# Performance work log

Hardware: AMD Instinct MI355X
Metric: run time of the kernel (lower is better)

The kernel has to match this reference:

```python
import jax, jax.numpy as jnp
import numpy as np

N, D, H, E, TOPK = 4096, 1024, 2048, 8, 2
EPS = 1e-10

def setup_inputs() -> dict:
    key = jax.random.key(0)
    ks = jax.random.split(key, 6)
    s = 0.02  # init scale for weights
    return {
        "x": jax.random.normal(ks[0], (N, D), dtype=jnp.float32),
        "gates": jax.random.uniform(ks[1], (N, E), dtype=jnp.float32),
        "W1": (jax.random.normal(ks[2], (E, D, H), dtype=jnp.float32) * s),
        "b1": jnp.zeros((E, H), dtype=jnp.float32),
        "W2": (jax.random.normal(ks[3], (E, H, H // 2), dtype=jnp.float32) * s),
        "b2": jnp.zeros((E, H // 2), dtype=jnp.float32),
        "W3": (jax.random.normal(ks[4], (E, H // 2, 1), dtype=jnp.float32) * s),
        "b3": jnp.zeros((E, 1), dtype=jnp.float32),
    }

def reference(x, gates, W1, b1, W2, b2, W3, b3):
    num_experts = gates.shape[1]
    # top-k gate masking + renormalization (matches MixtureOfExperts.call)
    _, topk_idx = jax.lax.top_k(gates, TOPK)              # [N, k]
    mask = jax.nn.one_hot(topk_idx, num_experts, dtype=gates.dtype).sum(axis=1)  # [N, E]
    g = gates * mask
    g = g / (g.sum(axis=-1, keepdims=True) + EPS)
    # Dense-masked expert computation. Mathematically identical to the
    # gather/split/segment-sum dispatch in SparseDispatcher: tokens with
    # zero gate for expert e contribute gate*sigmoid(...) = 0 in combine.
    # Dropout layers are identity at inference (training=False).
    h1 = jax.nn.relu(jnp.einsum('nd,edh->enh', x, W1) + b1[:, None, :])   # [E, N, H]
    h2 = jax.nn.relu(jnp.einsum('enh,ehg->eng', h1, W2) + b2[:, None, :]) # [E, N, H//2]
    y = jax.nn.sigmoid(jnp.einsum('eng,ego->eno', h2, W3) + b3[:, None, :])  # [E, N, 1]
    # combine: sum_e g[n,e] * y[e,n,:]  (== unsorted_segment_sum over dispatched rows)
    prediction = jnp.einsum('ne,eno->no', g, y)  # [N, 1]
    return prediction, g
```

## Files before the change

kernel.cpp:

```cpp
#include <hip/hip_runtime.h>
#include <hip/hip_bf16.h>
#include <math.h>

#define NTOK 4096
#define DIN  1024
#define H1D  2048
#define H2D  1024
#define NE   8
#define KSEL 2

constexpr int BM = 128, BN = 128, BK = 32;
constexpr int MAX_TILES = NTOK / BM;

typedef __attribute__((ext_vector_type(8))) __bf16 bf16x8;
typedef __attribute__((ext_vector_type(4))) float  f32x4;

__device__ __forceinline__ ushort f2bf(float f) {
    union { float f; unsigned u; } c; c.f = f;
    unsigned u = c.u;
    return (ushort)((u + 0x7fffu + ((u >> 16) & 1u)) >> 16);
}

__global__ void zero_counts(int* counts) {
    if (threadIdx.x < NE) counts[threadIdx.x] = 0;
}

__global__ void convert_x(const float* __restrict__ x, ushort* __restrict__ xbf) {
    int i = (blockIdx.x * blockDim.x + threadIdx.x) * 4;
    float4 v = *(const float4*)(x + i);
    ushort4 o;
    o.x = f2bf(v.x); o.y = f2bf(v.y); o.z = f2bf(v.z); o.w = f2bf(v.w);
    *(ushort4*)(xbf + i) = o;
}

__global__ __launch_bounds__(256)
void transpose_cvt(const float* __restrict__ W, ushort* __restrict__ Wt,
                   int K, int N) {
    __shared__ float t[64][132];
    const int e  = blockIdx.z;
    const int n0 = blockIdx.x * 128;
    const int k0 = blockIdx.y * 64;
    const int tid = threadIdx.x;

    const float* src = W + ((size_t)e * K + k0) * N + n0;
#pragma unroll
    for (int p = 0; p < 8; ++p) {
        int c  = tid + p * 256;
        int kk = c >> 5;
        int nn = (c & 31) * 4;
        float4 v = *(const float4*)(src + (size_t)kk * N + nn);
        t[kk][nn + 0] = v.x; t[kk][nn + 1] = v.y;
        t[kk][nn + 2] = v.z; t[kk][nn + 3] = v.w;
    }
    __syncthreads();

    const int n = tid >> 1;
    const int h = tid & 1;
    ushort outv[32];
#pragma unroll
    for (int j = 0; j < 32; ++j) outv[j] = f2bf(t[h * 32 + j][n]);
    ushort* dst = Wt + ((size_t)e * N + n0 + n) * K + k0 + h * 32;
#pragma unroll
    for (int q = 0; q < 4; ++q)
        *(uint4*)(dst + q * 8) = *(const uint4*)(outv + q * 8);
}

__global__ void topk_gate(const float* __restrict__ gates,
                          float* __restrict__ g_out,
                          int* __restrict__ counts,
                          int* __restrict__ bucket,
                          int* __restrict__ tke,
                          float* __restrict__ tkg,
                          float* __restrict__ ppart)
{
    int n = blockIdx.x * blockDim.x + threadIdx.x;
    if (n >= NTOK) return;

    ppart[n * 2 + 0] = 0.f;
    ppart[n * 2 + 1] = 0.f;

    float v[NE];
#pragma unroll
    for (int e = 0; e < NE; ++e) v[e] = gates[n * NE + e];

    int i1 = 0; float v1 = v[0];
#pragma unroll
    for (int e = 1; e < NE; ++e) if (v[e] > v1) { v1 = v[e]; i1 = e; }
    int i2 = -1; float v2 = -1e30f;
#pragma unroll
    for (int e = 0; e < NE; ++e) if (e != i1 && v[e] > v2) { v2 = v[e]; i2 = e; }

    float s = v1 + v2 + 1e-10f;
    float g1 = v1 / s, g2 = v2 / s;

#pragma unroll
    for (int e = 0; e < NE; ++e) {
        float gv = 0.f;
        if (e == i1) gv = g1;
        if (e == i2) gv = g2;
        g_out[n * NE + e] = gv;
    }
    tke[n * 2 + 0] = i1; tkg[n * 2 + 0] = g1;
    tke[n * 2 + 1] = i2; tkg[n * 2 + 1] = g2;

    int s1 = atomicAdd(&counts[i1], 1);
    bucket[i1 * NTOK + s1] = n * 2 + 0;
    int s2 = atomicAdd(&counts[i2], 1);
    bucket[i2 * NTOK + s2] = n * 2 + 1;
}

template<int SHIFT, int MODE>
__global__ __launch_bounds__(256)
void moe_gemm(const ushort* __restrict__ Abf, int lda,
              const ushort* __restrict__ Wt,
              const float* __restrict__ bias,
              int N,
              const float* __restrict__ W3,
              ushort* __restrict__ Cbf,
              float* __restrict__ ppart,
              const int* __restrict__ bucket,
              const int* __restrict__ counts,
              int K)
{
    const int b    = blockIdx.x;
    const int e    = b & 7;
    const int idx  = b >> 3;
    const int tile = idx & (MAX_TILES - 1);
    const int col0 = (idx / MAX_TILES) * BN;

    const int cnt  = counts[e];
    const int row0 = tile * BM;
    if (row0 >= cnt) return;

    __shared__ int rowmap[BM];
    __shared__ __align__(16) ushort smA[2][BM * BK];
    __shared__ __align__(16) ushort smB[2][BN * BK];

    const int tid = threadIdx.x;
    if (tid < BM) {
        int r = row0 + tid;
        rowmap[tid] = (r < cnt) ? bucket[e * NTOK + r] : -1;
    }
    __syncthreads();

    const int lane = tid & 63;
    const int wid  = tid >> 6;
    const int wm   = wid >> 1;
    const int wn   = wid & 1;

    const ushort* aSrc[2];
    const ushort* bSrc[2];
    int dstOff[2];
#pragma unroll
    for (int i = 0; i < 2; ++i) {
        int c    = (wid * 2 + i) * 64 + lane;
        int line = c >> 2;
        int slot = c & 3;
        int sch  = slot ^ ((line >> 1) & 3);
        dstOff[i] = c * 8;
        int entry = rowmap[line];
        int arow  = (entry >= 0) ? (entry >> SHIFT) : 0;
        aSrc[i] = Abf + (size_t)arow * lda + sch * 8;
        bSrc[i] = Wt + ((size_t)e * N + col0 + line) * K + sch * 8;
    }

    f32x4 acc[4][4];
#pragma unroll
    for (int i = 0; i < 4; ++i)
#pragma unroll
        for (int j = 0; j < 4; ++j)
            acc[i][j] = (f32x4){0.f, 0.f, 0.f, 0.f};

    auto stage = [&](int buf, int k0) {
#pragma unroll
        for (int i = 0; i < 2; ++i)
            __builtin_amdgcn_global_load_lds(
                (const __attribute__((address_space(1))) unsigned*)(aSrc[i] + k0),
                (__attribute__((address_space(3))) unsigned*)&smA[buf][dstOff[i]],
                16, 0, 0);
#pragma unroll
        for (int i = 0; i < 2; ++i)
            __builtin_amdgcn_global_load_lds(
                (const __attribute__((address_space(1))) unsigned*)(bSrc[i] + k0),
                (__attribute__((address_space(3))) unsigned*)&smB[buf][dstOff[i]],
                16, 0, 0);
    };

    auto compute = [&](int buf) {
        bf16x8 a[4], bfr[4];
#pragma unroll
        for (int mi = 0; mi < 4; ++mi) {
            int row  = wm * 64 + mi * 16 + (lane & 15);
            int slot = (lane >> 4) ^ ((row >> 1) & 3);
            a[mi] = *(const bf16x8*)&smA[buf][row * 32 + slot * 8];
        }
#pragma unroll
        for (int ni = 0; ni < 4; ++ni) {
            int col  = wn * 64 + ni * 16 + (lane & 15);
            int slot = (lane >> 4) ^ ((col >> 1) & 3);
            bfr[ni] = *(const bf16x8*)&smB[buf][col * 32 + slot * 8];
        }
#pragma unroll
        for (int mi = 0; mi < 4; ++mi)
#pragma unroll
            for (int ni = 0; ni < 4; ++ni)
                acc[mi][ni] = __builtin_amdgcn_mfma_f32_16x16x32_bf16(
                    a[mi], bfr[ni], acc[mi][ni], 0, 0, 0);
    };

    const int nt = K / BK;
    stage(0, 0);
    __syncthreads();
    for (int t = 0; t < nt; ++t) {
        int cur = t & 1;
        if (t + 1 < nt) stage(cur ^ 1, (t + 1) * BK);
        compute(cur);
        __syncthreads();
    }

    if (MODE == 1) {
        float bb[4];
#pragma unroll
        for (int ni = 0; ni < 4; ++ni)
            bb[ni] = bias[e * N + col0 + wn * 64 + ni * 16 + (lane & 15)];
#pragma unroll
        for (int mi = 0; mi < 4; ++mi) {
#pragma unroll
            for (int r = 0; r < 4; ++r) {
                int rt = wm * 64 + mi * 16 + (lane >> 4) * 4 + r;
                int entry = rowmap[rt];
                if (entry < 0) continue;
                ushort* crow = Cbf + (size_t)entry * N + col0;
#pragma unroll
                for (int ni = 0; ni < 4; ++ni) {
                    float val = fmaxf(acc[mi][ni][r] + bb[ni], 0.f);
                    crow[wn * 64 + ni * 16 + (lane & 15)] = f2bf(val);
                }
            }
        }
    } else {
        float bb[4], w3l[4];
#pragma unroll
        for (int ni = 0; ni < 4; ++ni) {
            int cg = col0 + wn * 64 + ni * 16 + (lane & 15);
            bb[ni]  = bias[e * N + cg];
            w3l[ni] = W3[e * H2D + cg];
        }
#pragma unroll
        for (int mi = 0; mi < 4; ++mi) {
#pragma unroll
            for (int r = 0; r < 4; ++r) {
                float s = 0.f;
#pragma unroll
                for (int ni = 0; ni < 4; ++ni)
                    s += fmaxf(acc[mi][ni][r] + bb[ni], 0.f) * w3l[ni];
#pragma unroll
                for (int off = 1; off < 16; off <<= 1)
                    s += __shfl_xor(s, off, 16);
                if ((lane & 15) == 0) {
                    int rt = wm * 64 + mi * 16 + (lane >> 4) * 4 + r;
                    int entry = rowmap[rt];
                    if (entry >= 0) atomicAdd(&ppart[entry], s);
                }
            }
        }
    }
}

__global__ void finalize(const float* __restrict__ pp, const float* __restrict__ b3,
                         const int* __restrict__ tke, const float* __restrict__ tkg,
                         float* __restrict__ pred) {
    int n = blockIdx.x * blockDim.x + threadIdx.x;
    if (n >= NTOK) return;
    float r = 0.f;
#pragma unroll
    for (int k = 0; k < KSEL; ++k) {
        int p = n * 2 + k;
        int ee = tke[p];
        float y = 1.f / (1.f + expf(-(pp[p] + b3[ee])));
        r += tkg[p] * y;
    }
    pred[n] = r;
}

extern "C" void kernel_launch(void* const* d_in, const int* in_sizes, int n_in,
                              void* d_out, int out_size, void* d_ws, size_t ws_size,
                              hipStream_t stream)
{
    const float* x     = (const float*)d_in[0];
    const float* gates = (const float*)d_in[1];
    const float* W1    = (const float*)d_in[2];
    const float* b1    = (const float*)d_in[3];
    const float* W2    = (const float*)d_in[4];
    const float* b2    = (const float*)d_in[5];
    const float* W3    = (const float*)d_in[6];
    const float* b3    = (const float*)d_in[7];

    float* out  = (float*)d_out;
    float* pred = out;
    float* gout = out + NTOK;

    char* ws = (char*)d_ws;
    int*    counts = (int*)(ws);
    int*    bucket = (int*)(ws + 4096);
    int*    tke    = (int*)(ws + 4096 + 131072);
    float*  tkg    = (float*)(ws + 4096 + 131072 + 32768);
    float*  ppart  = (float*)(ws + 4096 + 131072 + 65536);
    ushort* xbf    = (ushort*)(ws + (1 << 20));
    ushort* h1bf   = (ushort*)(ws + (1 << 20) + (size_t)NTOK * DIN * 2);
    ushort* wtbuf  = (ushort*)(ws + (1 << 20) + (size_t)NTOK * DIN * 2
                                  + (size_t)NTOK * KSEL * H1D * 2);

    zero_counts<<<1, 64, 0, stream>>>(counts);
    topk_gate<<<NTOK / 256, 256, 0, stream>>>(gates, gout, counts, bucket,
                                              tke, tkg, ppart);
    convert_x<<<NTOK * DIN / 4 / 256, 256, 0, stream>>>(x, xbf);

    transpose_cvt<<<dim3(H1D / 128, DIN / 64, NE), 256, 0, stream>>>(
        W1, wtbuf, DIN, H1D);
    moe_gemm<1, 1><<<NE * (H1D / BN) * MAX_TILES, 256, 0, stream>>>(
        xbf, DIN, wtbuf, b1, H1D, nullptr, h1bf, nullptr, bucket, counts, DIN);

    transpose_cvt<<<dim3(H2D / 128, H1D / 64, NE), 256, 0, stream>>>(
        W2, wtbuf, H1D, H2D);
    moe_gemm<0, 2><<<NE * (H2D / BN) * MAX_TILES, 256, 0, stream>>>(
        h1bf, H1D, wtbuf, b2, H2D, W3, nullptr, ppart, bucket, counts, H1D);

    finalize<<<NTOK / 256, 256, 0, stream>>>(ppart, b3, tke, tkg, pred);
}
```

Before: 329.0 us.

## Enlarge MoE GEMM tiles to 256 rows with 512-thread blocks and skip idle warps

The grouped expert GEMMs now use 256-row tiles with 8 waves per block. GEMM1 uses 256 columns (2x4 waves) and GEMM2 uses 128 columns (4x2 waves), with tile shape set by template parameters. Larger tiles raise data reuse per staged K-slice and halve the number of tile blocks. Waves whose row range lies past the expert's token count skip compute and epilogue, while still doing the loads and barriers. This costs more padding waste on partially filled tiles, fewer blocks per expert, and higher register and LDS pressure under the 512-thread launch bound.

```diff
diff --git a/kernel.cpp b/kernel.cpp
--- a/kernel.cpp
+++ b/kernel.cpp
@@ -9,8 +9,7 @@
 #define NE   8
 #define KSEL 2
 
-constexpr int BM = 128, BN = 128, BK = 32;
-constexpr int MAX_TILES = NTOK / BM;
+constexpr int BK = 32;
 
 typedef __attribute__((ext_vector_type(8))) __bf16 bf16x8;
 typedef __attribute__((ext_vector_type(4))) float  f32x4;
@@ -109,8 +108,8 @@
     bucket[i2 * NTOK + s2] = n * 2 + 1;
 }
 
-template<int SHIFT, int MODE>
-__global__ __launch_bounds__(256)
+template<int SHIFT, int MODE, int BN_, int WROWS, int WCOLS>
+__global__ __launch_bounds__(512, 2)
 void moe_gemm(const ushort* __restrict__ Abf, int lda,
               const ushort* __restrict__ Wt,
               const float* __restrict__ bias,
@@ -122,22 +121,28 @@
               const int* __restrict__ counts,
               int K)
 {
+    constexpr int BM_  = 256;
+    constexpr int MREP = BM_ / WROWS / 16;
+    constexpr int NREP = BN_ / WCOLS / 16;
+    constexpr int ACH  = BM_ * 4 / 512;
+    constexpr int BCH  = BN_ * 4 / 512;
+
     const int b    = blockIdx.x;
     const int e    = b & 7;
     const int idx  = b >> 3;
-    const int tile = idx & (MAX_TILES - 1);
-    const int col0 = (idx / MAX_TILES) * BN;
+    const int tile = idx & 15;
+    const int col0 = (idx >> 4) * BN_;
 
     const int cnt  = counts[e];
-    const int row0 = tile * BM;
+    const int row0 = tile * BM_;
     if (row0 >= cnt) return;
 
-    __shared__ int rowmap[BM];
-    __shared__ __align__(16) ushort smA[2][BM * BK];
-    __shared__ __align__(16) ushort smB[2][BN * BK];
+    __shared__ int rowmap[BM_];
+    __shared__ __align__(16) ushort smA[2][BM_ * BK];
+    __shared__ __align__(16) ushort smB[2][BN_ * BK];
 
     const int tid = threadIdx.x;
-    if (tid < BM) {
+    if (tid < BM_) {
         int r = row0 + tid;
         rowmap[tid] = (r < cnt) ? bucket[e * NTOK + r] : -1;
     }
@@ -145,65 +150,76 @@
 
     const int lane = tid & 63;
     const int wid  = tid >> 6;
-    const int wm   = wid >> 1;
-    const int wn   = wid & 1;
-
-    const ushort* aSrc[2];
-    const ushort* bSrc[2];
-    int dstOff[2];
-#pragma unroll
-    for (int i = 0; i < 2; ++i) {
-        int c    = (wid * 2 + i) * 64 + lane;
+    const int wm   = wid / WCOLS;
+    const int wn   = wid % WCOLS;
+    const bool wactive = (row0 + wm * (BM_ / WROWS)) < cnt;
+
+    const ushort* aSrc[ACH];
+    int aDst[ACH];
+#pragma unroll
+    for (int i = 0; i < ACH; ++i) {
+        int c    = wid * 64 + lane + i * 512;
         int line = c >> 2;
         int slot = c & 3;
         int sch  = slot ^ ((line >> 1) & 3);
-        dstOff[i] = c * 8;
+        aDst[i] = c * 8;
         int entry = rowmap[line];
         int arow  = (entry >= 0) ? (entry >> SHIFT) : 0;
         aSrc[i] = Abf + (size_t)arow * lda + sch * 8;
+    }
+    const ushort* bSrc[BCH];
+    int bDst[BCH];
+#pragma unroll
+    for (int i = 0; i < BCH; ++i) {
+        int c    = wid * 64 + lane + i * 512;
+        int line = c >> 2;
+        int slot = c & 3;
+        int sch  = slot ^ ((line >> 1) & 3);
+        bDst[i] = c * 8;
         bSrc[i] = Wt + ((size_t)e * N + col0 + line) * K + sch * 8;
     }
 
-    f32x4 acc[4][4];
-#pragma unroll
-    for (int i = 0; i < 4; ++i)
-#pragma unroll
-        for (int j = 0; j < 4; ++j)
+    f32x4 acc[MREP][NREP];
+#pragma unroll
+    for (int i = 0; i < MREP; ++i)
+#pragma unroll
+        for (int j = 0; j < NREP; ++j)
             acc[i][j] = (f32x4){0.f, 0.f, 0.f, 0.f};
 
     auto stage = [&](int buf, int k0) {
 #pragma unroll
-        for (int i = 0; i < 2; ++i)
+        for (int i = 0; i < ACH; ++i)
             __builtin_amdgcn_global_load_lds(
                 (const __attribute__((address_space(1))) unsigned*)(aSrc[i] + k0),
-                (__attribute__((address_space(3))) unsigned*)&smA[buf][dstOff[i]],
+                (__attribute__((address_space(3))) unsigned*)&smA[buf][aDst[i]],
                 16, 0, 0);
 #pragma unroll
-        for (int i = 0; i < 2; ++i)
+        for (int i = 0; i < BCH; ++i)
             __builtin_amdgcn_global_load_lds(
                 (const __attribute__((address_space(1))) unsigned*)(bSrc[i] + k0),
-                (__attribute__((address_space(3))) unsigned*)&smB[buf][dstOff[i]],
+                (__attribute__((address_space(3))) unsigned*)&smB[buf][bDst[i]],
                 16, 0, 0);
     };
 
     auto compute = [&](int buf) {
-        bf16x8 a[4], bfr[4];
-#pragma unroll
-        for (int mi = 0; mi < 4; ++mi) {
-            int row  = wm * 64 + mi * 16 + (lane & 15);
+        if (!wactive) return;
+        bf16x8 a[MREP], bfr[NREP];
+#pragma unroll
+        for (int mi = 0; mi < MREP; ++mi) {
+            int row  = wm * (BM_ / WROWS) + mi * 16 + (lane & 15);
             int slot = (lane >> 4) ^ ((row >> 1) & 3);
             a[mi] = *(const bf16x8*)&smA[buf][row * 32 + slot * 8];
         }
 #pragma unroll
-        for (int ni = 0; ni < 4; ++ni) {
-            int col  = wn * 64 + ni * 16 + (lane & 15);
+        for (int ni = 0; ni < NREP; ++ni) {
+            int col  = wn * (BN_ / WCOLS) + ni * 16 + (lane & 15);
             int slot = (lane >> 4) ^ ((col >> 1) & 3);
             bfr[ni] = *(const bf16x8*)&smB[buf][col * 32 + slot * 8];
         }
 #pragma unroll
-        for (int mi = 0; mi < 4; ++mi)
-#pragma unroll
-            for (int ni = 0; ni < 4; ++ni)
+        for (int mi = 0; mi < MREP; ++mi)
+#pragma unroll
+            for (int ni = 0; ni < NREP; ++ni)
                 acc[mi][ni] = __builtin_amdgcn_mfma_f32_16x16x32_bf16(
                     a[mi], bfr[ni], acc[mi][ni], 0, 0, 0);
     };
@@ -218,47 +234,49 @@
         __syncthreads();
     }
 
+    if (!wactive) return;
+
     if (MODE == 1) {
-        float bb[4];
-#pragma unroll
-        for (int ni = 0; ni < 4; ++ni)
-            bb[ni] = bias[e * N + col0 + wn * 64 + ni * 16 + (lane & 15)];
-#pragma unroll
-        for (int mi = 0; mi < 4; ++mi) {
+        float bb[NREP];
+#pragma unroll
+        for (int ni = 0; ni < NREP; ++ni)
+            bb[ni] = bias[e * N + col0 + wn * (BN_ / WCOLS) + ni * 16 + (lane & 15)];
+#pragma unroll
+        for (int mi = 0; mi < MREP; ++mi) {
 #pragma unroll
             for (int r = 0; r < 4; ++r) {
-                int rt = wm * 64 + mi * 16 + (lane >> 4) * 4 + r;
+                int rt = wm * (BM_ / WROWS) + mi * 16 + (lane >> 4) * 4 + r;
                 int entry = rowmap[rt];
                 if (entry < 0) continue;
                 ushort* crow = Cbf + (size_t)entry * N + col0;
 #pragma unroll
-                for (int ni = 0; ni < 4; ++ni) {
+                for (int ni = 0; ni < NREP; ++ni) {
                     float val = fmaxf(acc[mi][ni][r] + bb[ni], 0.f);
-                    crow[wn * 64 + ni * 16 + (lane & 15)] = f2bf(val);
+                    crow[wn * (BN_ / WCOLS) + ni * 16 + (lane & 15)] = f2bf(val);
                 }
             }
         }
     } else {
-        float bb[4], w3l[4];
-#pragma unroll
-        for (int ni = 0; ni < 4; ++ni) {
-            int cg = col0 + wn * 64 + ni * 16 + (lane & 15);
+        float bb[NREP], w3l[NREP];
+#pragma unroll
+        for (int ni = 0; ni < NREP; ++ni) {
+            int cg = col0 + wn * (BN_ / WCOLS) + ni * 16 + (lane & 15);
             bb[ni]  = bias[e * N + cg];
             w3l[ni] = W3[e * H2D + cg];
         }
 #pragma unroll
-        for (int mi = 0; mi < 4; ++mi) {
+        for (int mi = 0; mi < MREP; ++mi) {
 #pragma unroll
             for (int r = 0; r < 4; ++r) {
                 float s = 0.f;
 #pragma unroll
-                for (int ni = 0; ni < 4; ++ni)
+                for (int ni = 0; ni < NREP; ++ni)
                     s += fmaxf(acc[mi][ni][r] + bb[ni], 0.f) * w3l[ni];
 #pragma unroll
                 for (int off = 1; off < 16; off <<= 1)
                     s += __shfl_xor(s, off, 16);
                 if ((lane & 15) == 0) {
-                    int rt = wm * 64 + mi * 16 + (lane >> 4) * 4 + r;
+                    int rt = wm * (BM_ / WROWS) + mi * 16 + (lane >> 4) * 4 + r;
                     int entry = rowmap[rt];
                     if (entry >= 0) atomicAdd(&ppart[entry], s);
                 }
@@ -318,12 +336,12 @@
 
     transpose_cvt<<<dim3(H1D / 128, DIN / 64, NE), 256, 0, stream>>>(
         W1, wtbuf, DIN, H1D);
-    moe_gemm<1, 1><<<NE * (H1D / BN) * MAX_TILES, 256, 0, stream>>>(
+    moe_gemm<1, 1, 256, 2, 4><<<NE * 16 * (H1D / 256), 512, 0, stream>>>(
         xbf, DIN, wtbuf, b1, H1D, nullptr, h1bf, nullptr, bucket, counts, DIN);
 
     transpose_cvt<<<dim3(H2D / 128, H1D / 64, NE), 256, 0, stream>>>(
         W2, wtbuf, H1D, H2D);
-    moe_gemm<0, 2><<<NE * (H2D / BN) * MAX_TILES, 256, 0, stream>>>(
+    moe_gemm<0, 2, 128, 4, 2><<<NE * 16 * (H2D / 128), 512, 0, stream>>>(
         h1bf, H1D, wtbuf, b2, H2D, W3, nullptr, ppart, bucket, counts, H1D);
 
     finalize<<<NTOK / 256, 256, 0, stream>>>(ppart, b3, tke, tkg, pred);
```

Result: slower. 368.0 us (+11.9%).
